# Performance work log

Hardware: AMD Instinct MI355X
Metric: run time of the kernel (lower is better)

Reference implementation:

```python
import jax, jax.numpy as jnp
from jax import lax
import numpy as np

DN = ('NCHW', 'OIHW', 'NCHW')
EPS = 1e-5


def conv3(x, w, b=None):
    # 3x3 conv, stride 1, padding 1 (SAME)
    y = lax.conv_general_dilated(x, w, (1, 1), 'SAME', dimension_numbers=DN)
    return y if b is None else y + b[None, :, None, None]


def bn_relu(x, gamma, beta):
    # training-mode BatchNorm2d (batch statistics over N,H,W) + ReLU
    m = jnp.mean(x, axis=(0, 2, 3), keepdims=True)
    v = jnp.var(x, axis=(0, 2, 3), keepdims=True)
    y = (x - m) * lax.rsqrt(v + EPS)
    y = y * gamma[None, :, None, None] + beta[None, :, None, None]
    return jax.nn.relu(y)


def _w(key, o, i):
    # torch init: normal(0, sqrt(2/(k*k*out)))
    std = np.sqrt(2.0 / (3 * 3 * o))
    return jax.random.normal(key, (o, i, 3, 3), dtype=jnp.float32) * std


def setup_inputs() -> dict:
    key = jax.random.key(0)
    ks = jax.random.split(key, 16)
    C = 256
    Ch = C // 2
    B, H, W = 4, 160, 160
    d = {}
    d['fpn_fea'] = jax.random.normal(ks[0], (B, C, H, W), dtype=jnp.float32)
    # sc_smooth_layer: conv(C->C)+BN+ReLU, conv(C->C/2)+BN+ReLU (no conv bias)
    d['w_sc1'] = _w(ks[1], C, C); d['g_sc1'] = jnp.ones((C,)); d['b_sc1'] = jnp.zeros((C,))
    d['w_sc2'] = _w(ks[2], Ch, C); d['g_sc2'] = jnp.ones((Ch,)); d['b_sc2'] = jnp.zeros((Ch,))
    # shrink / centroid heads: plain conv(C/2 -> 1) with bias
    d['w_shrink'] = _w(ks[3], 1, Ch); d['bias_shrink'] = jnp.zeros((1,))
    d['w_cent'] = _w(ks[4], 1, Ch); d['bias_cent'] = jnp.zeros((1,))
    # param_head
    d['w_p1'] = _w(ks[5], C, C); d['g_p1'] = jnp.ones((C,)); d['b_p1'] = jnp.zeros((C,))
    d['w_p2'] = _w(ks[6], Ch, C); d['g_p2'] = jnp.ones((Ch,)); d['b_p2'] = jnp.zeros((Ch,))
    d['w_p3'] = _w(ks[7], 2, Ch); d['bias_p3'] = jnp.zeros((2,))
    # shift_head
    d['w_s1'] = _w(ks[8], C, C); d['g_s1'] = jnp.ones((C,)); d['b_s1'] = jnp.zeros((C,))
    d['w_s2'] = _w(ks[9], Ch, C); d['g_s2'] = jnp.ones((Ch,)); d['b_s2'] = jnp.zeros((Ch,))
    d['w_s3'] = _w(ks[10], 8, Ch); d['bias_s3'] = jnp.zeros((8,))
    return d


def reference(fpn_fea, w_sc1, g_sc1, b_sc1, w_sc2, g_sc2, b_sc2,
              w_shrink, bias_shrink, w_cent, bias_cent,
              w_p1, g_p1, b_p1, w_p2, g_p2, b_p2, w_p3, bias_p3,
              w_s1, g_s1, b_s1, w_s2, g_s2, b_s2, w_s3, bias_s3):
    smooth = bn_relu(conv3(fpn_fea, w_sc1), g_sc1, b_sc1)
    smooth = bn_relu(conv3(smooth, w_sc2), g_sc2, b_sc2)
    shrink = conv3(smooth, w_shrink, bias_shrink)      # [B,1,H,W]
    centroid = conv3(smooth, w_cent, bias_cent)        # [B,1,H,W]
    p = bn_relu(conv3(fpn_fea, w_p1), g_p1, b_p1)
    p = bn_relu(conv3(p, w_p2), g_p2, b_p2)
    param = conv3(p, w_p3, bias_p3)                    # [B,2,H,W]
    s = bn_relu(conv3(fpn_fea, w_s1), g_s1, b_s1)
    s = bn_relu(conv3(s, w_s2), g_s2, b_s2)
    shift = conv3(s, w_s3, bias_s3)                    # [B,8,H,W]
    return (shrink, centroid, param, shift)
```

## Files before the change

### kernel.cpp

```cpp
#include <hip/hip_runtime.h>

typedef short bf16x8 __attribute__((ext_vector_type(8)));
typedef float f32x4 __attribute__((ext_vector_type(4)));

__device__ __forceinline__ float bf2f(unsigned short u) {
    union { unsigned int i; float f; } c; c.i = ((unsigned int)u) << 16; return c.f;
}
__device__ __forceinline__ unsigned short f2bf(float f) {
    union { float f; unsigned int i; } c; c.f = f;
    unsigned int u = c.i;
    u += 0x7fffu + ((u >> 16) & 1u);
    return (unsigned short)(u >> 16);
}

__device__ __forceinline__ void gload_lds16(const unsigned short* g, unsigned short* l) {
    __builtin_amdgcn_global_load_lds(
        (const __attribute__((address_space(1))) void*)g,
        (__attribute__((address_space(3))) void*)l, 16, 0, 0);
}


__device__ __forceinline__ void zero_border_one(unsigned short* buf, int C, int idx) {
    int CV = C >> 3;
    int cv = idx % CV; int t = idx / CV;
    int p = t % 644;   int n = t / 644;
    int h, w;
    if (p < 162)      { h = 0;   w = p; }
    else if (p < 324) { h = 161; w = p - 162; }
    else { int q = p - 324; h = 1 + (q >> 1); w = (q & 1) ? 161 : 0; }
    uint4 z = make_uint4(0u, 0u, 0u, 0u);
    *(uint4*)(buf + ((size_t)((n * 162 + h) * 162) + w) * C + cv * 8) = z;
}

__device__ __forceinline__ void do_zero(unsigned short* xpad,
                                        unsigned short* buf1, size_t s1,
                                        unsigned short* buf2, size_t s2, int nbr, int idx) {
    if (idx < 82432) { zero_border_one(xpad, 256, idx); return; }
    idx -= 82432;
    int nb1 = nbr * 82432;
    if (idx < nb1) { zero_border_one(buf1 + (size_t)(idx / 82432) * s1, 256, idx % 82432); return; }
    idx -= nb1;
    int nb2 = nbr * 41216;
    if (idx < nb2) { zero_border_one(buf2 + (size_t)(idx / 41216) * s2, 128, idx % 41216); }
}

__device__ __forceinline__ void do_transpose(const float* __restrict__ x,
                                             unsigned short* __restrict__ xpad, int idx) {
    int w = idx % 160; int t = idx / 160;
    int cv = t % 32;   t /= 32;
    int h = t % 160;   int n = t / 160;
    const float* src = x + (((size_t)(n * 256 + cv * 8) * 160 + h) * 160 + w);
    unsigned short us[8];
#pragma unroll
    for (int k = 0; k < 8; ++k) us[k] = f2bf(src[(size_t)k * 25600]);
    uint4 o;
    o.x = (unsigned int)us[0] | ((unsigned int)us[1] << 16);
    o.y = (unsigned int)us[2] | ((unsigned int)us[3] << 16);
    o.z = (unsigned int)us[4] | ((unsigned int)us[5] << 16);
    o.w = (unsigned int)us[6] | ((unsigned int)us[7] << 16);
    *(uint4*)(xpad + ((size_t)((n * 162 + h + 1) * 162) + (w + 1)) * 256 + cv * 8) = o;
}

__device__ __forceinline__ void do_pack(const float* s0, const float* s1, const float* s2,
                                        const float* s3, const float* s4, const float* s5,
                                        unsigned short* w1p, unsigned short* w2p, int idx) {
    int t = idx / 294912, r = idx - t * 294912;
    const float* src; unsigned short* dst; int coBase;
    if (t < 6) {
        int br = t >> 1;
        src = (br == 0) ? s0 : (br == 1) ? s1 : s2;
        coBase = (t & 1) * 128;
        dst = w1p + (size_t)t * 294912;
    } else {
        int br = t - 6;
        src = (br == 0) ? s3 : (br == 1) ? s4 : s5;
        coBase = 0;
        dst = w2p + (size_t)br * 294912;
    }
    int tap, ci, o;
    if (r < 262144) {
        int tp = r >> 16, rem = r & 65535;
        int q = rem >> 13, r2 = rem & 8191;
        int e = r2 & 7, gco = r2 >> 3;
        int co = gco & 127, g = gco >> 7;
        tap = tp * 2 + (g >> 2);
        ci = q * 32 + (g & 3) * 8 + e;
        o = coBase + co;
    } else {
        int rem = r - 262144;
        int q = rem >> 12, r2 = rem & 4095;
        int e = r2 & 7, gco = r2 >> 3;
        int co = gco & 127, g = gco >> 7;
        tap = 8;
        ci = q * 32 + g * 8 + e;
        o = coBase + co;
    }
    dst[r] = f2bf(src[((size_t)(o * 256 + ci)) * 9 + tap]);
}

__global__ void prep(const float* __restrict__ fpn, unsigned short* __restrict__ xpad,
                     unsigned short* __restrict__ buf1, size_t s1,
                     unsigned short* __restrict__ buf2, size_t s2, int nbr,
                     int zb, int zcount, float* __restrict__ stats,
                     const float* w10, const float* w11, const float* w12,
                     const float* w20, const float* w21, const float* w22,
                     unsigned short* __restrict__ w1p, unsigned short* __restrict__ w2p) {
    int bid = blockIdx.x;
    if (bid < 3) {
        ((float4*)stats)[bid * 256 + threadIdx.x] = make_float4(0.f, 0.f, 0.f, 0.f);
        return;
    }
    bid -= 3;
    if (bid < zb) {
        int idx = bid * 256 + threadIdx.x;
        if (idx < zcount) do_zero(xpad, buf1, s1, buf2, s2, nbr, idx);
        return;
    }
    bid -= zb;
    if (bid < 12800) { do_transpose(fpn, xpad, bid * 256 + threadIdx.x); return; }
    bid -= 12800;
    do_pack(w10, w11, w12, w20, w21, w22, w1p, w2p, bid * 256 + threadIdx.x);
}

template<int COT, int BPB>
__global__ __launch_bounds__(256, 2) void conv3x3_mfma(
        const unsigned short* __restrict__ xpad0, size_t xstride,
        const unsigned short* __restrict__ wpk0, size_t wstride,
        unsigned short* __restrict__ ypad0, size_t ystride,
        float* __restrict__ stats, int sstride) {
    __shared__ __align__(16) unsigned short As[16384];
    __shared__ __align__(16) unsigned short Bs[12288];

    const int br = blockIdx.x / BPB;
    int bid = blockIdx.x % BPB;
    const unsigned short* xpad = xpad0 + (size_t)br * xstride;
    const unsigned short* wpk  = wpk0 + (size_t)br * wstride;
    unsigned short* ypad       = ypad0 + (size_t)br * ystride;
    float* sum   = stats + (size_t)br * sstride;
    float* sumsq = sum + 256;

    const int tid = threadIdx.x;
    const int wv = tid >> 6, lane = tid & 63;
    const int quad = lane >> 4, l15 = lane & 15;
    const int wco = wv >> 1, wsp = wv & 1;

    const int wt = bid % 5;
    const int ht = (bid / 5) % 20;
    const int n = (bid / 100) % 4;
    const int tile = bid / 400;
    const int co0 = tile * 128;
    const int h0 = ht * 8, w0 = wt * 32;

    const unsigned short* wtile = wpk + (size_t)tile * 294912;

    int boff[6];
#pragma unroll
    for (int r = 0; r < 6; ++r) {
        int slot = r * 256 + tid;
        int g = slot / 384, p = slot - g * 384;
        if (p > 339) p = 339;
        int prow = p / 34, pcol = p - prow * 34;
        boff[r] = ((n * 162 + h0 + prow) * 162 + (w0 + pcol)) * 256 + g * 8;
    }

    int p0[8];
#pragma unroll
    for (int j = 0; j < 8; ++j) {
        int sp = wsp * 128 + j * 16 + l15;
        p0[j] = (sp >> 5) * 34 + (sp & 31);
    }

    f32x4 acc[4][8];
#pragma unroll
    for (int i = 0; i < 4; ++i)
#pragma unroll
        for (int j = 0; j < 8; ++j) acc[i][j] = (f32x4){0.f, 0.f, 0.f, 0.f};

    for (int q = 0; q < 8; ++q) {
#pragma unroll
        for (int w = 0; w < 3; ++w) {
            __syncthreads();
            if (w == 0) {
                const unsigned short* bq = xpad + q * 32;
#pragma unroll
                for (int r = 0; r < 6; ++r)
                    gload_lds16(bq + boff[r], (unsigned short*)Bs + (r * 256 + tid) * 8);
            }
            if (w < 2) {
#pragma unroll
                for (int h = 0; h < 2; ++h) {
                    const unsigned short* asrc = wtile + (w * 2 + h) * 65536 + q * 8192 + tid * 8;
#pragma unroll
                    for (int c = 0; c < 4; ++c)
                        gload_lds16(asrc + c * 2048,
                                    (unsigned short*)As + h * 8192 + c * 2048 + tid * 8);
                }
            } else {
                const unsigned short* asrc = wtile + 262144 + q * 4096 + tid * 8;
#pragma unroll
                for (int c = 0; c < 2; ++c)
                    gload_lds16(asrc + c * 2048, (unsigned short*)As + c * 2048 + tid * 8);
            }
            __syncthreads();

#pragma unroll
            for (int t = 0; t < 4; ++t) {
                if (w == 2 && t >= 1) continue;
                const int TAP = (w < 2) ? (w * 4 + t) : 8;
                const int dh = TAP / 3, dw = TAP % 3;
                const int toff = dh * 34 + dw;
                const int g0 = (w < 2) ? ((t & 1) * 4 + quad) : quad;
                const unsigned short* Ab = As + ((w < 2) ? (t >> 1) * 8192 : 0);
                bf16x8 a[4];
#pragma unroll
                for (int i = 0; i < 4; ++i)
                    a[i] = *(const bf16x8*)(Ab + (size_t)(g0 * 128 + wco * 64 + i * 16 + l15) * 8);
#pragma unroll
                for (int jh = 0; jh < 2; ++jh) {
                    bf16x8 b[4];
#pragma unroll
                    for (int j = 0; j < 4; ++j)
                        b[j] = *(const bf16x8*)(Bs + (size_t)(quad * 384 + p0[jh * 4 + j] + toff) * 8);
#pragma unroll
                    for (int i = 0; i < 4; ++i)
#pragma unroll
                        for (int j = 0; j < 4; ++j)
                            acc[i][jh * 4 + j] = __builtin_amdgcn_mfma_f32_16x16x32_bf16(
                                a[i], b[j], acc[i][jh * 4 + j], 0, 0, 0);
                }
            }
        }
    }

#pragma unroll
    for (int i = 0; i < 4; ++i) {
        const int co_l = wco * 64 + i * 16 + quad * 4;
#pragma unroll
        for (int j = 0; j < 8; ++j) {
            const int sp = wsp * 128 + j * 16 + l15;
            const int jh = sp >> 5, jw = sp & 31;
            f32x4 v = acc[i][j];
            ushort4 pk;
            pk.x = f2bf(v[0]); pk.y = f2bf(v[1]); pk.z = f2bf(v[2]); pk.w = f2bf(v[3]);
            *(ushort4*)(ypad + ((size_t)((n * 162 + h0 + jh + 1) * 162) + (w0 + jw + 1)) * COT
                        + co0 + co_l) = pk;
        }
#pragma unroll
        for (int r = 0; r < 4; ++r) {
            float s1 = 0.f, s2 = 0.f;
#pragma unroll
            for (int j = 0; j < 8; ++j) { float v = acc[i][j][r]; s1 += v; s2 += v * v; }
#pragma unroll
            for (int m = 1; m < 16; m <<= 1) {
                s1 += __shfl_xor(s1, m, 64);
                s2 += __shfl_xor(s2, m, 64);
            }
            if (l15 == 0) {
                atomicAdd(&sum[co0 + co_l + r], s1);
                atomicAdd(&sumsq[co0 + co_l + r], s2);
            }
        }
    }
}

template<int C, int BPB>
__global__ void bn_apply(unsigned short* __restrict__ buf0, size_t bstride,
                         const float* __restrict__ stats, int sstride,
                         const float* g0, const float* g1, const float* g2,
                         const float* be0, const float* be1, const float* be2) {
    const int br = blockIdx.x / BPB;
    unsigned short* buf = buf0 + (size_t)br * bstride;
    const float* sum = stats + (size_t)br * sstride;
    const float* sumsq = sum + 256;
    const float* gamma = (br == 0) ? g0 : (br == 1) ? g1 : g2;
    const float* beta  = (br == 0) ? be0 : (br == 1) ? be1 : be2;

    __shared__ float s_sc[C], s_sh[C];
    if (threadIdx.x < C) {
        int c = threadIdx.x;
        const float inv = 1.0f / 102400.0f;
        float m = sum[c] * inv;
        float v = sumsq[c] * inv - m * m;
        float sc = gamma[c] * rsqrtf(v + 1e-5f);
        s_sc[c] = sc;
        s_sh[c] = beta[c] - m * sc;
    }
    __syncthreads();

    constexpr int CV = C / 8;
    int idx = (blockIdx.x % BPB) * 256 + threadIdx.x;
    int cv = idx % CV; int pos = idx / CV;
    int w = pos % 160; int h = (pos / 160) % 160; int n = pos / 25600;
    unsigned short* p = buf + ((size_t)((n * 162 + h + 1) * 162) + (w + 1)) * C + cv * 8;
    uint4 v = *(const uint4*)p;
    unsigned int ua[4] = {v.x, v.y, v.z, v.w};
    unsigned int ob[4];
#pragma unroll
    for (int j = 0; j < 4; ++j) {
        int c = cv * 8 + j * 2;
        float f0 = bf2f((unsigned short)(ua[j] & 0xffffu)) * s_sc[c] + s_sh[c];
        float f1 = bf2f((unsigned short)(ua[j] >> 16)) * s_sc[c + 1] + s_sh[c + 1];
        f0 = fmaxf(f0, 0.f); f1 = fmaxf(f1, 0.f);
        ob[j] = (unsigned int)f2bf(f0) | ((unsigned int)f2bf(f1) << 16);
    }
    uint4 o = make_uint4(ob[0], ob[1], ob[2], ob[3]);
    *(uint4*)p = o;
}

__global__ __launch_bounds__(256) void heads_all(
        const unsigned short* __restrict__ zb, size_t zstride,
        const float* __restrict__ stats2, int sstride,
        const float* g20, const float* g21, const float* g22,
        const float* be20, const float* be21, const float* be22,
        const float* w_sh, const float* bi_sh, const float* w_ce, const float* bi_ce,
        const float* w_p3, const float* bi_p3, const float* w_s3, const float* bi_s3,
        float* __restrict__ out) {
    const int br = blockIdx.x / 400;
    const int bid = blockIdx.x % 400;
    const unsigned short* z = zb + (size_t)br * zstride;
    const float* sum   = stats2 + (size_t)br * sstride;
    const float* sumsq = sum + 256;
    const float* gamma = (br == 0) ? g20 : (br == 1) ? g21 : g22;
    const float* beta  = (br == 0) ? be20 : (br == 1) ? be21 : be22;

    __shared__ float s_sc[128], s_sh[128];
    __shared__ float s_w[8 * 9 * 128];
    __shared__ __align__(16) unsigned short s_z[1536 * 8];

    const int tid = threadIdx.x;
    if (tid < 128) {
        const float inv = 1.0f / 102400.0f;
        float m = sum[tid] * inv;
        float v = sumsq[tid] * inv - m * m;
        float sc = gamma[tid] * rsqrtf(v + 1e-5f);
        s_sc[tid] = sc;
        s_sh[tid] = beta[tid] - m * sc;
    }
    if (br == 0) {
        for (int t = tid; t < 2 * 1152; t += 256) {
            int ci = t % 128; int r = t / 128;
            int tap = r % 9;  int which = r / 9;
            const float* src = which ? w_ce : w_sh;
            s_w[t] = src[(size_t)ci * 9 + tap];
        }
    } else {
        const float* wsrc = (br == 1) ? w_p3 : w_s3;
        const int nco = (br == 1) ? 2 : 8;
        for (int t = tid; t < nco * 1152; t += 256) {
            int ci = t % 128; int r = t / 128;
            int tap = r % 9;  int o = r / 9;
            s_w[t] = wsrc[((size_t)(o * 128 + ci)) * 9 + tap];
        }
    }

    const int wt = bid % 5, ht = (bid / 5) % 20, n = bid / 100;
    const int h0 = ht * 8, w0 = wt * 32;

    int zoff[6];
#pragma unroll
    for (int r = 0; r < 6; ++r) {
        int slot = r * 256 + tid;
        if (slot > 1359) slot = 1359;
        int c8 = slot / 340, pos = slot - c8 * 340;
        int prow = pos / 34, pcol = pos - prow * 34;
        zoff[r] = ((n * 162 + h0 + prow) * 162 + (w0 + pcol)) * 128 + c8 * 8;
    }
    const int prow_t = tid >> 5, pcol_t = tid & 31;

    float acc[8];
#pragma unroll
    for (int o = 0; o < 8; ++o) acc[o] = 0.f;

    for (int ph = 0; ph < 4; ++ph) {
        __syncthreads();
#pragma unroll
        for (int r = 0; r < 6; ++r)
            gload_lds16(z + zoff[r] + ph * 32, (unsigned short*)s_z + (r * 256 + tid) * 8);
        __syncthreads();

#pragma unroll
        for (int dh = 0; dh < 3; ++dh)
#pragma unroll
            for (int dw = 0; dw < 3; ++dw) {
                const int tap = dh * 3 + dw;
                const int pos = (prow_t + dh) * 34 + pcol_t + dw;
                const int hh = h0 + prow_t + dh, ww = w0 + pcol_t + dw;
                const bool edge = (hh == 0) | (hh == 161) | (ww == 0) | (ww == 161);
#pragma unroll
                for (int c8 = 0; c8 < 4; ++c8) {
                    uint4 v = *(const uint4*)(s_z + (size_t)(c8 * 340 + pos) * 8);
                    unsigned int ua[4] = {v.x, v.y, v.z, v.w};
                    float zv[8];
#pragma unroll
                    for (int j = 0; j < 4; ++j) {
                        int c = ph * 32 + c8 * 8 + 2 * j;
                        float x0 = bf2f((unsigned short)(ua[j] & 0xffffu));
                        float x1 = bf2f((unsigned short)(ua[j] >> 16));
                        float y0 = fmaxf(x0 * s_sc[c] + s_sh[c], 0.f);
                        float y1 = fmaxf(x1 * s_sc[c + 1] + s_sh[c + 1], 0.f);
                        zv[2 * j]     = edge ? 0.f : y0;
                        zv[2 * j + 1] = edge ? 0.f : y1;
                    }
                    if (br == 0) {
                        const float* wp1 = &s_w[tap * 128 + ph * 32 + c8 * 8];
                        const float* wp2 = &s_w[1152 + tap * 128 + ph * 32 + c8 * 8];
#pragma unroll
                        for (int e = 0; e < 8; ++e) {
                            acc[0] = fmaf(zv[e], wp1[e], acc[0]);
                            acc[1] = fmaf(zv[e], wp2[e], acc[1]);
                        }
                    } else if (br == 1) {
#pragma unroll
                        for (int o = 0; o < 2; ++o) {
                            const float* wp = &s_w[(o * 9 + tap) * 128 + ph * 32 + c8 * 8];
#pragma unroll
                            for (int e = 0; e < 8; ++e)
                                acc[o] = fmaf(zv[e], wp[e], acc[o]);
                        }
                    } else {
#pragma unroll
                        for (int o = 0; o < 8; ++o) {
                            const float* wp = &s_w[(o * 9 + tap) * 128 + ph * 32 + c8 * 8];
#pragma unroll
                            for (int e = 0; e < 8; ++e)
                                acc[o] = fmaf(zv[e], wp[e], acc[o]);
                        }
                    }
                }
            }
    }
    const int pw = w0 + pcol_t, phh = h0 + prow_t;
    if (br == 0) {
        out[(size_t)n * 25600 + phh * 160 + pw] = acc[0] + bi_sh[0];
        out[102400 + (size_t)n * 25600 + phh * 160 + pw] = acc[1] + bi_ce[0];
    } else if (br == 1) {
#pragma unroll
        for (int o = 0; o < 2; ++o)
            out[204800 + ((size_t)(n * 2 + o)) * 25600 + phh * 160 + pw] = acc[o] + bi_p3[o];
    } else {
#pragma unroll
        for (int o = 0; o < 8; ++o)
            out[409600 + ((size_t)(n * 8 + o)) * 25600 + phh * 160 + pw] = acc[o] + bi_s3[o];
    }
}

template<int CO>
__global__ __launch_bounds__(256) void head_conv(const unsigned short* __restrict__ z,
                                                 const float* __restrict__ w,
                                                 const float* __restrict__ bias,
                                                 float* __restrict__ out) {
    __shared__ float s_w[CO * 9 * 128];
    for (int t = threadIdx.x; t < CO * 9 * 128; t += 256) {
        int ci = t % 128; int r = t / 128;
        int tap = r % 9;  int o = r / 9;
        s_w[t] = w[((size_t)(o * 128 + ci)) * 9 + tap];
    }
    __syncthreads();
    const int pos = blockIdx.x * 256 + threadIdx.x;
    const int pw = pos % 160, ph = (pos / 160) % 160, pn = pos / 25600;
    float acc[CO];
#pragma unroll
    for (int o = 0; o < CO; ++o) acc[o] = bias[o];
#pragma unroll
    for (int dh = 0; dh < 3; ++dh)
#pragma unroll
        for (int dw = 0; dw < 3; ++dw) {
            const int tap = dh * 3 + dw;
            const unsigned short* zp = z + ((size_t)((pn * 162 + ph + dh) * 162) + (pw + dw)) * 128;
            for (int c8 = 0; c8 < 16; ++c8) {
                uint4 v = *(const uint4*)(zp + c8 * 8);
                unsigned int ua[4] = {v.x, v.y, v.z, v.w};
                float xv[8];
#pragma unroll
                for (int j = 0; j < 4; ++j) {
                    xv[2 * j]     = bf2f((unsigned short)(ua[j] & 0xffffu));
                    xv[2 * j + 1] = bf2f((unsigned short)(ua[j] >> 16));
                }
#pragma unroll
                for (int o = 0; o < CO; ++o) {
                    const float* wp = &s_w[(o * 9 + tap) * 128 + c8 * 8];
#pragma unroll
                    for (int e = 0; e < 8; ++e) acc[o] = fmaf(xv[e], wp[e], acc[o]);
                }
            }
        }
#pragma unroll
    for (int o = 0; o < CO; ++o)
        out[((size_t)(pn * CO + o)) * 25600 + ph * 160 + pw] = acc[o];
}

__global__ __launch_bounds__(256) void head_conv_dual(const unsigned short* __restrict__ z,
                                                      const float* __restrict__ w1, const float* __restrict__ b1,
                                                      const float* __restrict__ w2, const float* __restrict__ b2,
                                                      float* __restrict__ out1, float* __restrict__ out2) {
    __shared__ float s_w[2 * 9 * 128];
    for (int t = threadIdx.x; t < 2 * 9 * 128; t += 256) {
        int ci = t % 128; int r = t / 128;
        int tap = r % 9;  int which = r / 9;
        const float* src = which ? w2 : w1;
        s_w[t] = src[(size_t)ci * 9 + tap];
    }
    __syncthreads();
    const int pos = blockIdx.x * 256 + threadIdx.x;
    const int pw = pos % 160, ph = (pos / 160) % 160, pn = pos / 25600;
    float a1 = b1[0], a2 = b2[0];
#pragma unroll
    for (int dh = 0; dh < 3; ++dh)
#pragma unroll
        for (int dw = 0; dw < 3; ++dw) {
            const int tap = dh * 3 + dw;
            const unsigned short* zp = z + ((size_t)((pn * 162 + ph + dh) * 162) + (pw + dw)) * 128;
            for (int c8 = 0; c8 < 16; ++c8) {
                uint4 v = *(const uint4*)(zp + c8 * 8);
                unsigned int ua[4] = {v.x, v.y, v.z, v.w};
                float xv[8];
#pragma unroll
                for (int j = 0; j < 4; ++j) {
                    xv[2 * j]     = bf2f((unsigned short)(ua[j] & 0xffffu));
                    xv[2 * j + 1] = bf2f((unsigned short)(ua[j] >> 16));
                }
                const float* wp1 = &s_w[tap * 128 + c8 * 8];
                const float* wp2 = &s_w[1152 + tap * 128 + c8 * 8];
#pragma unroll
                for (int e = 0; e < 8; ++e) {
                    a1 = fmaf(xv[e], wp1[e], a1);
                    a2 = fmaf(xv[e], wp2[e], a2);
                }
            }
        }
    out1[(size_t)pn * 25600 + ph * 160 + pw] = a1;
    out2[(size_t)pn * 25600 + ph * 160 + pw] = a2;
}

extern "C" void kernel_launch(void* const* d_in, const int* in_sizes, int n_in,
                              void* d_out, int out_size, void* d_ws, size_t ws_size,
                              hipStream_t stream) {
    const float* fpn = (const float*)d_in[0];
    const float* W1[3] = {(const float*)d_in[1],  (const float*)d_in[11], (const float*)d_in[19]};
    const float* G1[3] = {(const float*)d_in[2],  (const float*)d_in[12], (const float*)d_in[20]};
    const float* B1[3] = {(const float*)d_in[3],  (const float*)d_in[13], (const float*)d_in[21]};
    const float* W2[3] = {(const float*)d_in[4],  (const float*)d_in[14], (const float*)d_in[22]};
    const float* G2[3] = {(const float*)d_in[5],  (const float*)d_in[15], (const float*)d_in[23]};
    const float* B2[3] = {(const float*)d_in[6],  (const float*)d_in[16], (const float*)d_in[24]};
    const float* w_shrink = (const float*)d_in[7];  const float* b_shrink = (const float*)d_in[8];
    const float* w_cent   = (const float*)d_in[9];  const float* b_cent   = (const float*)d_in[10];
    const float* w_p3     = (const float*)d_in[17]; const float* b_p3     = (const float*)d_in[18];
    const float* w_s3     = (const float*)d_in[25]; const float* b_s3     = (const float*)d_in[26];
    float* out = (float*)d_out;

    const size_t S1 = (size_t)4 * 162 * 162 * 256;
    const size_t S2 = (size_t)4 * 162 * 162 * 128;
    const size_t need_fused = S1 * 2 * 4 + S2 * 2 * 3
                              + (size_t)9 * 294912 * 2 + 6 * 512 * 4;

    char* ws = (char*)d_ws;
    size_t off = 0;
    unsigned short* xpad = (unsigned short*)(ws + off); off += S1 * 2;
    const int NBR = (ws_size >= need_fused) ? 3 : 1;
    unsigned short* buf1 = (unsigned short*)(ws + off); off += S1 * 2 * NBR;
    unsigned short* buf2 = (unsigned short*)(ws + off); off += S2 * 2 * NBR;
    unsigned short* w1p  = (unsigned short*)(ws + off); off += (size_t)6 * 294912 * 2;
    unsigned short* w2p  = (unsigned short*)(ws + off); off += (size_t)3 * 294912 * 2;
    float* stats         = (float*)(ws + off);          off += (size_t)6 * 512 * 4;

    {
        int zcount = 82432 * (1 + NBR) + 41216 * NBR;
        int zb = (zcount + 255) / 256;
        prep<<<3 + zb + 12800 + 10368, 256, 0, stream>>>(
            fpn, xpad, buf1, S1, buf2, S2, NBR, zb, zcount, stats,
            W1[0], W1[1], W1[2], W2[0], W2[1], W2[2], w1p, w2p);
    }

    if (NBR == 3) {
        conv3x3_mfma<256, 800><<<2400, 256, 0, stream>>>(
            xpad, 0, w1p, (size_t)2 * 294912, buf1, S1, stats, 1024);
        bn_apply<256, 12800><<<38400, 256, 0, stream>>>(
            buf1, S1, stats, 1024, G1[0], G1[1], G1[2], B1[0], B1[1], B1[2]);
        conv3x3_mfma<128, 400><<<1200, 256, 0, stream>>>(
            buf1, S1, w2p, (size_t)294912, buf2, S2, stats + 512, 1024);
        heads_all<<<1200, 256, 0, stream>>>(
            buf2, S2, stats + 512, 1024,
            G2[0], G2[1], G2[2], B2[0], B2[1], B2[2],
            w_shrink, b_shrink, w_cent, b_cent, w_p3, b_p3, w_s3, b_s3, out);
    } else {
        for (int br = 0; br < 3; ++br) {
            conv3x3_mfma<256, 800><<<800, 256, 0, stream>>>(
                xpad, 0, w1p + (size_t)br * 2 * 294912, 0, buf1, 0, stats + br * 1024, 0);
            bn_apply<256, 12800><<<12800, 256, 0, stream>>>(
                buf1, 0, stats + br * 1024, 0, G1[br], G1[br], G1[br], B1[br], B1[br], B1[br]);
            conv3x3_mfma<128, 400><<<400, 256, 0, stream>>>(
                buf1, 0, w2p + (size_t)br * 294912, 0, buf2, 0, stats + 512 + br * 1024, 0);
            bn_apply<128, 6400><<<6400, 256, 0, stream>>>(
                buf2, 0, stats + 512 + br * 1024, 0, G2[br], G2[br], G2[br], B2[br], B2[br], B2[br]);
            if (br == 0) {
                head_conv_dual<<<400, 256, 0, stream>>>(buf2, w_shrink, b_shrink, w_cent, b_cent,
                                                        out, out + 102400);
            } else if (br == 1) {
                head_conv<2><<<400, 256, 0, stream>>>(buf2, w_p3, b_p3, out + 204800);
            } else {
                head_conv<8><<<400, 256, 0, stream>>>(buf2, w_s3, b_s3, out + 409600);
            }
        }
    }
}
```

Measured before the change: 1.147 ms.

## Fuse first BatchNorm+ReLU into second conv's input staging

Removes the separate bn_apply pass over the three 256-channel intermediate buffers. The second conv now reads raw conv1 output with ordinary register loads, applies the per-channel scale/shift and ReLU, zeroes padding-border pixels, and writes the result to LDS. Because the border is forced to zero in the kernel, prep no longer clears the borders of buf1/buf2. This saves a full read-modify-write of roughly 80MB of bf16 data. In exchange, the activation loads go through registers instead of direct global-to-LDS transfers, and the conv inner loop does extra ALU work per tile.

```diff
diff --git a/kernel.cpp b/kernel.cpp
--- a/kernel.cpp
+++ b/kernel.cpp
@@ -100,7 +100,7 @@
 
 __global__ void prep(const float* __restrict__ fpn, unsigned short* __restrict__ xpad,
                      unsigned short* __restrict__ buf1, size_t s1,
-                     unsigned short* __restrict__ buf2, size_t s2, int nbr,
+                     unsigned short* __restrict__ buf2, size_t s2, int zeroNbr,
                      int zb, int zcount, float* __restrict__ stats,
                      const float* w10, const float* w11, const float* w12,
                      const float* w20, const float* w21, const float* w22,
@@ -113,7 +113,7 @@
     bid -= 3;
     if (bid < zb) {
         int idx = bid * 256 + threadIdx.x;
-        if (idx < zcount) do_zero(xpad, buf1, s1, buf2, s2, nbr, idx);
+        if (idx < zcount) do_zero(xpad, buf1, s1, buf2, s2, zeroNbr, idx);
         return;
     }
     bid -= zb;
@@ -215,6 +215,192 @@
 #pragma unroll
                 for (int i = 0; i < 4; ++i)
                     a[i] = *(const bf16x8*)(Ab + (size_t)(g0 * 128 + wco * 64 + i * 16 + l15) * 8);
+#pragma unroll
+                for (int jh = 0; jh < 2; ++jh) {
+                    bf16x8 b[4];
+#pragma unroll
+                    for (int j = 0; j < 4; ++j)
+                        b[j] = *(const bf16x8*)(Bs + (size_t)(quad * 384 + p0[jh * 4 + j] + toff) * 8);
+#pragma unroll
+                    for (int i = 0; i < 4; ++i)
+#pragma unroll
+                        for (int j = 0; j < 4; ++j)
+                            acc[i][jh * 4 + j] = __builtin_amdgcn_mfma_f32_16x16x32_bf16(
+                                a[i], b[j], acc[i][jh * 4 + j], 0, 0, 0);
+                }
+            }
+        }
+    }
+
+#pragma unroll
+    for (int i = 0; i < 4; ++i) {
+        const int co_l = wco * 64 + i * 16 + quad * 4;
+#pragma unroll
+        for (int j = 0; j < 8; ++j) {
+            const int sp = wsp * 128 + j * 16 + l15;
+            const int jh = sp >> 5, jw = sp & 31;
+            f32x4 v = acc[i][j];
+            ushort4 pk;
+            pk.x = f2bf(v[0]); pk.y = f2bf(v[1]); pk.z = f2bf(v[2]); pk.w = f2bf(v[3]);
+            *(ushort4*)(ypad + ((size_t)((n * 162 + h0 + jh + 1) * 162) + (w0 + jw + 1)) * COT
+                        + co0 + co_l) = pk;
+        }
+#pragma unroll
+        for (int r = 0; r < 4; ++r) {
+            float s1 = 0.f, s2 = 0.f;
+#pragma unroll
+            for (int j = 0; j < 8; ++j) { float v = acc[i][j][r]; s1 += v; s2 += v * v; }
+#pragma unroll
+            for (int m = 1; m < 16; m <<= 1) {
+                s1 += __shfl_xor(s1, m, 64);
+                s2 += __shfl_xor(s2, m, 64);
+            }
+            if (l15 == 0) {
+                atomicAdd(&sum[co0 + co_l + r], s1);
+                atomicAdd(&sumsq[co0 + co_l + r], s2);
+            }
+        }
+    }
+}
+
+template<int COT, int BPB>
+__global__ __launch_bounds__(256, 2) void conv3x3_bnfused(
+        const unsigned short* __restrict__ xpad0, size_t xstride,
+        const unsigned short* __restrict__ wpk0, size_t wstride,
+        unsigned short* __restrict__ ypad0, size_t ystride,
+        float* __restrict__ stats2, int sstride2,
+        const float* __restrict__ stats1, int sstride1,
+        const float* g0, const float* g1, const float* g2,
+        const float* be0, const float* be1, const float* be2) {
+    __shared__ __align__(16) unsigned short As[16384];
+    __shared__ __align__(16) unsigned short Bs[12288];
+    __shared__ float s_sc[256], s_sh[256];
+
+    const int br = blockIdx.x / BPB;
+    int bid = blockIdx.x % BPB;
+    const unsigned short* xpad = xpad0 + (size_t)br * xstride;
+    const unsigned short* wpk  = wpk0 + (size_t)br * wstride;
+    unsigned short* ypad       = ypad0 + (size_t)br * ystride;
+    float* sum   = stats2 + (size_t)br * sstride2;
+    float* sumsq = sum + 256;
+    const float* sum1   = stats1 + (size_t)br * sstride1;
+    const float* sumsq1 = sum1 + 256;
+    const float* gamma = (br == 0) ? g0 : (br == 1) ? g1 : g2;
+    const float* beta  = (br == 0) ? be0 : (br == 1) ? be1 : be2;
+
+    const int tid = threadIdx.x;
+    {
+        const float inv = 1.0f / 102400.0f;
+        float m = sum1[tid] * inv;
+        float v = sumsq1[tid] * inv - m * m;
+        float sc = gamma[tid] * rsqrtf(v + 1e-5f);
+        s_sc[tid] = sc;
+        s_sh[tid] = beta[tid] - m * sc;
+    }
+
+    const int wv = tid >> 6, lane = tid & 63;
+    const int quad = lane >> 4, l15 = lane & 15;
+    const int wco = wv >> 1, wsp = wv & 1;
+
+    const int wt = bid % 5;
+    const int ht = (bid / 5) % 20;
+    const int n = (bid / 100) % 4;
+    const int tile = bid / 400;
+    const int co0 = tile * 128;
+    const int h0 = ht * 8, w0 = wt * 32;
+
+    const unsigned short* wtile = wpk + (size_t)tile * 294912;
+
+    int boff[6], gch[6];
+    bool bedge[6];
+#pragma unroll
+    for (int r = 0; r < 6; ++r) {
+        int slot = r * 256 + tid;
+        int g = slot / 384, p = slot - g * 384;
+        if (p > 339) p = 339;
+        int prow = p / 34, pcol = p - prow * 34;
+        boff[r] = ((n * 162 + h0 + prow) * 162 + (w0 + pcol)) * 256 + g * 8;
+        gch[r] = g * 8;
+        int hh = h0 + prow, ww = w0 + pcol;
+        bedge[r] = (hh == 0) | (hh == 161) | (ww == 0) | (ww == 161);
+    }
+
+    int p0[8];
+#pragma unroll
+    for (int j = 0; j < 8; ++j) {
+        int sp = wsp * 128 + j * 16 + l15;
+        p0[j] = (sp >> 5) * 34 + (sp & 31);
+    }
+
+    f32x4 acc[4][8];
+#pragma unroll
+    for (int i = 0; i < 4; ++i)
+#pragma unroll
+        for (int j = 0; j < 8; ++j) acc[i][j] = (f32x4){0.f, 0.f, 0.f, 0.f};
+
+    for (int q = 0; q < 8; ++q) {
+#pragma unroll
+        for (int w = 0; w < 3; ++w) {
+            __syncthreads();
+            if (w == 0) {
+                const unsigned short* bq = xpad + q * 32;
+                uint4 raw[6];
+#pragma unroll
+                for (int r = 0; r < 6; ++r)
+                    raw[r] = *(const uint4*)(bq + boff[r]);
+#pragma unroll
+                for (int h = 0; h < 2; ++h) {
+                    const unsigned short* asrc = wtile + h * 65536 + q * 8192 + tid * 8;
+#pragma unroll
+                    for (int c = 0; c < 4; ++c)
+                        gload_lds16(asrc + c * 2048,
+                                    (unsigned short*)As + h * 8192 + c * 2048 + tid * 8);
+                }
+#pragma unroll
+                for (int r = 0; r < 6; ++r) {
+                    unsigned int ua[4] = {raw[r].x, raw[r].y, raw[r].z, raw[r].w};
+                    unsigned int ob[4];
+                    const int cb = q * 32 + gch[r];
+#pragma unroll
+                    for (int j = 0; j < 4; ++j) {
+                        int c = cb + 2 * j;
+                        float f0 = fmaxf(bf2f((unsigned short)(ua[j] & 0xffffu)) * s_sc[c] + s_sh[c], 0.f);
+                        float f1 = fmaxf(bf2f((unsigned short)(ua[j] >> 16)) * s_sc[c + 1] + s_sh[c + 1], 0.f);
+                        if (bedge[r]) { f0 = 0.f; f1 = 0.f; }
+                        ob[j] = (unsigned int)f2bf(f0) | ((unsigned int)f2bf(f1) << 16);
+                    }
+                    *(uint4*)((unsigned short*)Bs + (r * 256 + tid) * 8) =
+                        make_uint4(ob[0], ob[1], ob[2], ob[3]);
+                }
+            } else if (w == 1) {
+#pragma unroll
+                for (int h = 0; h < 2; ++h) {
+                    const unsigned short* asrc = wtile + (2 + h) * 65536 + q * 8192 + tid * 8;
+#pragma unroll
+                    for (int c = 0; c < 4; ++c)
+                        gload_lds16(asrc + c * 2048,
+                                    (unsigned short*)As + h * 8192 + c * 2048 + tid * 8);
+                }
+            } else {
+                const unsigned short* asrc = wtile + 262144 + q * 4096 + tid * 8;
+#pragma unroll
+                for (int c = 0; c < 2; ++c)
+                    gload_lds16(asrc + c * 2048, (unsigned short*)As + c * 2048 + tid * 8);
+            }
+            __syncthreads();
+
+#pragma unroll
+            for (int t = 0; t < 4; ++t) {
+                if (w == 2 && t >= 1) continue;
+                const int TAP = (w < 2) ? (w * 4 + t) : 8;
+                const int dh = TAP / 3, dw = TAP % 3;
+                const int toff = dh * 34 + dw;
+                const int g0i = (w < 2) ? ((t & 1) * 4 + quad) : quad;
+                const unsigned short* Ab = As + ((w < 2) ? (t >> 1) * 8192 : 0);
+                bf16x8 a[4];
+#pragma unroll
+                for (int i = 0; i < 4; ++i)
+                    a[i] = *(const bf16x8*)(Ab + (size_t)(g0i * 128 + wco * 64 + i * 16 + l15) * 8);
 #pragma unroll
                 for (int jh = 0; jh < 2; ++jh) {
                     bf16x8 b[4];
@@ -563,26 +749,29 @@
     unsigned short* w2p  = (unsigned short*)(ws + off); off += (size_t)3 * 294912 * 2;
     float* stats         = (float*)(ws + off);          off += (size_t)6 * 512 * 4;
 
-    {
+    if (NBR == 3) {
+        int zcount = 82432;
+        int zb = (zcount + 255) / 256;
+        prep<<<3 + zb + 12800 + 10368, 256, 0, stream>>>(
+            fpn, xpad, buf1, S1, buf2, S2, 0, zb, zcount, stats,
+            W1[0], W1[1], W1[2], W2[0], W2[1], W2[2], w1p, w2p);
+
+        conv3x3_mfma<256, 800><<<2400, 256, 0, stream>>>(
+            xpad, 0, w1p, (size_t)2 * 294912, buf1, S1, stats, 1024);
+        conv3x3_bnfused<128, 400><<<1200, 256, 0, stream>>>(
+            buf1, S1, w2p, (size_t)294912, buf2, S2,
+            stats + 512, 1024, stats, 1024,
+            G1[0], G1[1], G1[2], B1[0], B1[1], B1[2]);
+        heads_all<<<1200, 256, 0, stream>>>(
+            buf2, S2, stats + 512, 1024,
+            G2[0], G2[1], G2[2], B2[0], B2[1], B2[2],
+            w_shrink, b_shrink, w_cent, b_cent, w_p3, b_p3, w_s3, b_s3, out);
+    } else {
         int zcount = 82432 * (1 + NBR) + 41216 * NBR;
         int zb = (zcount + 255) / 256;
         prep<<<3 + zb + 12800 + 10368, 256, 0, stream>>>(
             fpn, xpad, buf1, S1, buf2, S2, NBR, zb, zcount, stats,
             W1[0], W1[1], W1[2], W2[0], W2[1], W2[2], w1p, w2p);
-    }
-
-    if (NBR == 3) {
-        conv3x3_mfma<256, 800><<<2400, 256, 0, stream>>>(
-            xpad, 0, w1p, (size_t)2 * 294912, buf1, S1, stats, 1024);
-        bn_apply<256, 12800><<<38400, 256, 0, stream>>>(
-            buf1, S1, stats, 1024, G1[0], G1[1], G1[2], B1[0], B1[1], B1[2]);
-        conv3x3_mfma<128, 400><<<1200, 256, 0, stream>>>(
-            buf1, S1, w2p, (size_t)294912, buf2, S2, stats + 512, 1024);
-        heads_all<<<1200, 256, 0, stream>>>(
-            buf2, S2, stats + 512, 1024,
-            G2[0], G2[1], G2[2], B2[0], B2[1], B2[2],
-            w_shrink, b_shrink, w_cent, b_cent, w_p3, b_p3, w_s3, b_s3, out);
-    } else {
         for (int br = 0; br < 3; ++br) {
             conv3x3_mfma<256, 800><<<800, 256, 0, stream>>>(
                 xpad, 0, w1p + (size_t)br * 2 * 294912, 0, buf1, 0, stats + br * 1024, 0);
```

New measurement: 1.286 ms. 12.2% more time.
